# Performance work log

Hardware: AMD Instinct MI355X
Metric: run time of the kernel (lower is better)

Reference implementation:

```python
import jax, jax.numpy as jnp
import numpy as np

BYTE = 0xFF  # module operates on byte tensors; mask keeps int32 faithful to uint8 semantics

def _xnor(a, b):
    return (~(a ^ b)) & BYTE

def _swap(a):
    # cat((a[:, mid:], a[:, :mid]), dim=1)
    mid = a.shape[-1] // 2
    return jnp.concatenate([a[:, mid:], a[:, :mid]], axis=1)

def _transpose2(a):
    # view(B, W//2, 2) -> transpose(1,2) -> view(B, W): de-interleave even/odd lanes
    B, W = a.shape
    return a.reshape(B, W // 2, 2).transpose(0, 2, 1).reshape(B, W)

def _gen_rand_bits(key, shape):
    # (torch.rand(shape)*2).byte()*255 -> each byte is 0 or 255
    return jax.random.bernoulli(key, 0.5, shape).astype(jnp.int32) * 255

def setup_inputs() -> dict:
    key = jax.random.key(0)
    kx, k1, k2, k3, k4 = jax.random.split(key, 5)
    B, W = 8192, 8192
    x = jax.random.randint(kx, (B, W), 0, 256, dtype=jnp.int32)
    return {
        "x": x,
        "w1": _gen_rand_bits(k1, (W,)),
        "w2": _gen_rand_bits(k2, (W,)),
        "b1": _gen_rand_bits(k3, (W,)),
        "b2": _gen_rand_bits(k4, (W,)),
    }

def reference(x, w1, w2, b1, b2):
    z = _xnor(x, w1)          # b_xnor(x, w1)
    z = z & b1                # b_and(z, b1)
    z = _swap(z)
    x = x | z                 # b_or(x, z)
    x = _transpose2(x)
    z = _xnor(x, w2)          # b_xnor(x, w2)
    z = z | b2                # b_or(z, b2)
    z = _swap(z)
    x = x & z                 # b_and(x, z)
    x = _transpose2(x)
    return x
```

## Files before the change

### kernel.cpp

```cpp
#include <hip/hip_runtime.h>


constexpr int W     = 8192;
constexpr int WORDS = 2048;
constexpr int HALF  = 1024;
constexpr int RPB   = 4;

typedef unsigned u32;
typedef u32 u32x4 __attribute__((ext_vector_type(4)));

static __device__ __forceinline__ u32 perm_b32(u32 hi, u32 lo, u32 sel) {
    return __builtin_amdgcn_perm(hi, lo, sel);
}

static __device__ __forceinline__ u32 pack4(uint4 v) {
    return (v.x & 0xFFu) | ((v.y & 0xFFu) << 8) | ((v.z & 0xFFu) << 16) | ((v.w & 0xFFu) << 24);
}

static __device__ __forceinline__ void nt_store4(int* p, u32 packed) {
    u32x4 v = { packed & 0xFFu, (packed >> 8) & 0xFFu,
                (packed >> 16) & 0xFFu, packed >> 24 };
    __builtin_nontemporal_store(v, (u32x4*)p);
}

__global__ __launch_bounds__(256)
void residual_binary_kernel(const int* __restrict__ x,
                            const int* __restrict__ w1, const int* __restrict__ w2,
                            const int* __restrict__ b1, const int* __restrict__ b2,
                            int* __restrict__ out)
{
    __shared__ u32 Xs[WORDS];
    __shared__ u32 Ts[2][WORDS];

    const int t = threadIdx.x;

    u32 B1p[4][2], C1p[4][2], M2p[4][2], C2p[4][2];
#pragma unroll
    for (int q = 0; q < 4; ++q) {
        const int m = (2 * t + 512 * q) ^ HALF;
#pragma unroll
        for (int j = 0; j < 2; ++j) {
            const int e = 4 * (m + j);
            u32 pb1 = pack4(*(const uint4*)(b1 + e));
            u32 pw1 = pack4(*(const uint4*)(w1 + e));
            u32 pb2 = pack4(*(const uint4*)(b2 + e));
            u32 pw2 = pack4(*(const uint4*)(w2 + e));
            B1p[q][j] = pb1;
            C1p[q][j] = (~pw1) & pb1;
            M2p[q][j] = ~pb2;
            C2p[q][j] = ((~pw2) & (~pb2)) | pb2;
        }
    }

    const u32 sel_even = 0x06040200u;
    const u32 sel_odd  = 0x07050301u;

    const long long row0 = (long long)blockIdx.x * RPB;

    uint4 P[8];
    {
        const int* xr = x + row0 * (long long)W;
#pragma unroll
        for (int i = 0; i < 8; ++i)
            P[i] = *(const uint4*)(xr + 4 * (t + 256 * i));
    }

#pragma unroll
    for (int r = 0; r < RPB; ++r) {
        const int buf = r & 1;
        int* orow = out + (row0 + r) * (long long)W;

#pragma unroll
        for (int i = 0; i < 8; ++i)
            Xs[t + 256 * i] = pack4(P[i]);

        if (r + 1 < RPB) {
            const int* xn = x + (row0 + r + 1) * (long long)W;
#pragma unroll
            for (int i = 0; i < 8; ++i)
                P[i] = *(const uint4*)(xn + 4 * (t + 256 * i));
        }

        __syncthreads();

#pragma unroll
        for (int q = 0; q < 4; ++q) {
            const int m = 2 * t + 512 * q;
            uint2 xa = *(const uint2*)&Xs[m];
            uint2 xs = *(const uint2*)&Xs[m ^ HALF];
            u32 y0 = xa.x | ((xs.x & B1p[q][0]) ^ C1p[q][0]);
            u32 y1 = xa.y | ((xs.y & B1p[q][1]) ^ C1p[q][1]);
            const int K = t + 256 * q;
            Ts[buf][K]        = perm_b32(y1, y0, sel_even);
            Ts[buf][K + HALF] = perm_b32(y1, y0, sel_odd);
        }

        __syncthreads();

#pragma unroll
        for (int q = 0; q < 4; ++q) {
            const int m = 2 * t + 512 * q;
            uint2 ta = *(const uint2*)&Ts[buf][m];
            uint2 ts = *(const uint2*)&Ts[buf][m ^ HALF];
            u32 u0 = ta.x & ((ts.x & M2p[q][0]) ^ C2p[q][0]);
            u32 u1 = ta.y & ((ts.y & M2p[q][1]) ^ C2p[q][1]);
            const int K = t + 256 * q;
            nt_store4(orow + 4 * K,          perm_b32(u1, u0, sel_even));
            nt_store4(orow + 4 * (K + HALF), perm_b32(u1, u0, sel_odd));
        }
    }
}

extern "C" void kernel_launch(void* const* d_in, const int* in_sizes, int n_in,
                              void* d_out, int out_size, void* d_ws, size_t ws_size,
                              hipStream_t stream) {
    const int* x  = (const int*)d_in[0];
    const int* w1 = (const int*)d_in[1];
    const int* w2 = (const int*)d_in[2];
    const int* b1 = (const int*)d_in[3];
    const int* b2 = (const int*)d_in[4];
    int* out = (int*)d_out;

    const int rows = in_sizes[0] / W;
    const int grid = rows / RPB;
    residual_binary_kernel<<<grid, 256, 0, stream>>>(x, w1, w2, b1, b2, out);
}
```

Baseline: 89.06 us.

## Keep swap partners in registers, drop X shared buffer and one barrier

Changes the x load mapping so each thread loads both halves of its words (q and q^2), so the first half-swap is done from registers. This removes the Xs shared array, its stores and loads, and one __syncthreads per row. The second stage reads each Ts word once and takes the swapped partner from registers. The last row's prefetch now uses nontemporal loads. Each thread's global load pattern is now less interleaved across the block, which could affect coalescing.

New measurement: 85.11 us (median of 2 runs). 1.05x faster.

```diff
diff --git a/kernel.cpp b/kernel.cpp
--- a/kernel.cpp
+++ b/kernel.cpp
@@ -13,8 +13,8 @@
     return __builtin_amdgcn_perm(hi, lo, sel);
 }
 
-static __device__ __forceinline__ u32 pack4(uint4 v) {
-    return (v.x & 0xFFu) | ((v.y & 0xFFu) << 8) | ((v.z & 0xFFu) << 16) | ((v.w & 0xFFu) << 24);
+static __device__ __forceinline__ u32 pack4(u32x4 v) {
+    return (v[0] & 0xFFu) | ((v[1] & 0xFFu) << 8) | ((v[2] & 0xFFu) << 16) | ((v[3] & 0xFFu) << 24);
 }
 
 static __device__ __forceinline__ void nt_store4(int* p, u32 packed) {
@@ -29,26 +29,21 @@
                             const int* __restrict__ b1, const int* __restrict__ b2,
                             int* __restrict__ out)
 {
-    __shared__ u32 Xs[WORDS];
     __shared__ u32 Ts[2][WORDS];
-
     const int t = threadIdx.x;
 
-    u32 B1p[4][2], C1p[4][2], M2p[4][2], C2p[4][2];
+    u32 B1w[4][2], C1w[4][2], M2w[4][2], C2w[4][2];
 #pragma unroll
     for (int q = 0; q < 4; ++q) {
-        const int m = (2 * t + 512 * q) ^ HALF;
+        const int e = 4 * (2 * t + 512 * q);
 #pragma unroll
         for (int j = 0; j < 2; ++j) {
-            const int e = 4 * (m + j);
-            u32 pb1 = pack4(*(const uint4*)(b1 + e));
-            u32 pw1 = pack4(*(const uint4*)(w1 + e));
-            u32 pb2 = pack4(*(const uint4*)(b2 + e));
-            u32 pw2 = pack4(*(const uint4*)(w2 + e));
-            B1p[q][j] = pb1;
-            C1p[q][j] = (~pw1) & pb1;
-            M2p[q][j] = ~pb2;
-            C2p[q][j] = ((~pw2) & (~pb2)) | pb2;
+            u32 pb1 = pack4(*(const u32x4*)(b1 + e + 4 * j));
+            u32 pw1 = pack4(*(const u32x4*)(w1 + e + 4 * j));
+            u32 pb2 = pack4(*(const u32x4*)(b2 + e + 4 * j));
+            u32 pw2 = pack4(*(const u32x4*)(w2 + e + 4 * j));
+            B1w[q][j] = pb1;  C1w[q][j] = (~pw1) & pb1;
+            M2w[q][j] = ~pb2; C2w[q][j] = ((~pw2) & (~pb2)) | pb2;
         }
     }
 
@@ -57,12 +52,12 @@
 
     const long long row0 = (long long)blockIdx.x * RPB;
 
-    uint4 P[8];
+    u32x4 P[8];
     {
         const int* xr = x + row0 * (long long)W;
 #pragma unroll
-        for (int i = 0; i < 8; ++i)
-            P[i] = *(const uint4*)(xr + 4 * (t + 256 * i));
+        for (int k = 0; k < 8; ++k)
+            P[k] = *(const u32x4*)(xr + 8 * t + 2048 * (k >> 1) + 4 * (k & 1));
     }
 
 #pragma unroll
@@ -70,26 +65,32 @@
         const int buf = r & 1;
         int* orow = out + (row0 + r) * (long long)W;
 
+        u32 X[4][2];
 #pragma unroll
-        for (int i = 0; i < 8; ++i)
-            Xs[t + 256 * i] = pack4(P[i]);
+        for (int q = 0; q < 4; ++q) {
+            X[q][0] = pack4(P[2 * q]);
+            X[q][1] = pack4(P[2 * q + 1]);
+        }
 
         if (r + 1 < RPB) {
             const int* xn = x + (row0 + r + 1) * (long long)W;
+            if (r + 1 == 3) {
 #pragma unroll
-            for (int i = 0; i < 8; ++i)
-                P[i] = *(const uint4*)(xn + 4 * (t + 256 * i));
+                for (int k = 0; k < 8; ++k)
+                    P[k] = __builtin_nontemporal_load(
+                        (const u32x4*)(xn + 8 * t + 2048 * (k >> 1) + 4 * (k & 1)));
+            } else {
+#pragma unroll
+                for (int k = 0; k < 8; ++k)
+                    P[k] = *(const u32x4*)(xn + 8 * t + 2048 * (k >> 1) + 4 * (k & 1));
+            }
         }
-
-        __syncthreads();
 
 #pragma unroll
         for (int q = 0; q < 4; ++q) {
-            const int m = 2 * t + 512 * q;
-            uint2 xa = *(const uint2*)&Xs[m];
-            uint2 xs = *(const uint2*)&Xs[m ^ HALF];
-            u32 y0 = xa.x | ((xs.x & B1p[q][0]) ^ C1p[q][0]);
-            u32 y1 = xa.y | ((xs.y & B1p[q][1]) ^ C1p[q][1]);
+            const int p = q ^ 2;
+            u32 y0 = X[q][0] | ((X[p][0] & B1w[p][0]) ^ C1w[p][0]);
+            u32 y1 = X[q][1] | ((X[p][1] & B1w[p][1]) ^ C1w[p][1]);
             const int K = t + 256 * q;
             Ts[buf][K]        = perm_b32(y1, y0, sel_even);
             Ts[buf][K + HALF] = perm_b32(y1, y0, sel_odd);
@@ -97,13 +98,17 @@
 
         __syncthreads();
 
+        u32 Ta[4][2];
 #pragma unroll
         for (int q = 0; q < 4; ++q) {
-            const int m = 2 * t + 512 * q;
-            uint2 ta = *(const uint2*)&Ts[buf][m];
-            uint2 ts = *(const uint2*)&Ts[buf][m ^ HALF];
-            u32 u0 = ta.x & ((ts.x & M2p[q][0]) ^ C2p[q][0]);
-            u32 u1 = ta.y & ((ts.y & M2p[q][1]) ^ C2p[q][1]);
+            uint2 v = *(const uint2*)&Ts[buf][2 * t + 512 * q];
+            Ta[q][0] = v.x;  Ta[q][1] = v.y;
+        }
+#pragma unroll
+        for (int q = 0; q < 4; ++q) {
+            const int p = q ^ 2;
+            u32 u0 = Ta[q][0] & ((Ta[p][0] & M2w[p][0]) ^ C2w[p][0]);
+            u32 u1 = Ta[q][1] & ((Ta[p][1] & M2w[p][1]) ^ C2w[p][1]);
             const int K = t + 256 * q;
             nt_store4(orow + 4 * K,          perm_b32(u1, u0, sel_even));
             nt_store4(orow + 4 * (K + HALF), perm_b32(u1, u0, sel_odd));
```
